# Kernel tuning notes

Hardware: AMD Instinct MI355X
Metric: run time of the kernel (lower is better)

## Reference

```python
import jax, jax.numpy as jnp
import numpy as np

D_MODEL, D_STATE, D_CONV, EXPAND, DT_RANK = 1024, 16, 4, 2, 64
D_INNER = EXPAND * D_MODEL
B, L = 2, 4096


def setup_inputs() -> dict:
    key = jax.random.key(0)
    ks = jax.random.split(key, 9)
    s = 0.02
    x = jax.random.normal(ks[0], (B, L, D_MODEL), dtype=jnp.float32)
    in_proj_w = jax.random.normal(ks[1], (D_MODEL, 2 * D_INNER), dtype=jnp.float32) * s
    conv_w = jax.random.normal(ks[2], (D_INNER, 1, D_CONV), dtype=jnp.float32) * s
    conv_b = jnp.zeros((D_INNER,), dtype=jnp.float32)
    x_proj_w = jax.random.normal(ks[3], (D_INNER, DT_RANK + 2 * D_STATE), dtype=jnp.float32) * s
    dt_proj_w = jax.random.normal(ks[4], (DT_RANK, D_INNER), dtype=jnp.float32) * s
    # dt bias -> softplus(dt) roughly in [1e-3, 1e-1] as in mamba init
    dt = jnp.exp(jax.random.uniform(ks[5], (D_INNER,)) * (np.log(0.1) - np.log(1e-3)) + np.log(1e-3))
    dt_proj_b = (dt + jnp.log(-jnp.expm1(-dt))).astype(jnp.float32)  # inverse softplus
    A_log = jnp.log(jnp.broadcast_to(jnp.arange(1, D_STATE + 1, dtype=jnp.float32), (D_INNER, D_STATE)))
    Dp = jnp.ones((D_INNER,), dtype=jnp.float32)
    out_proj_w = jax.random.normal(ks[6], (D_INNER, D_MODEL), dtype=jnp.float32) * s
    return {"x": x, "in_proj_w": in_proj_w, "conv_w": conv_w, "conv_b": conv_b,
            "x_proj_w": x_proj_w, "dt_proj_w": dt_proj_w, "dt_proj_b": dt_proj_b,
            "A_log": A_log, "Dp": Dp, "out_proj_w": out_proj_w}


def _mamba(x, in_proj_w, conv_w, conv_b, x_proj_w, dt_proj_w, dt_proj_b, A_log, Dp, out_proj_w):
    # in projection -> (u, z), each [B, L, D_INNER]
    xz = jnp.einsum('bld,de->ble', x, in_proj_w)
    u, z = jnp.split(xz, 2, axis=-1)
    # causal depthwise conv1d over time
    u_c = jax.lax.conv_general_dilated(
        u.transpose(0, 2, 1), conv_w, window_strides=(1,),
        padding=[(D_CONV - 1, 0)],
        dimension_numbers=('NCH', 'OIH', 'NCH'),
        feature_group_count=D_INNER)
    u_c = jax.nn.silu(u_c.transpose(0, 2, 1) + conv_b)  # [B, L, D_INNER]
    # input-dependent dt, B, C
    dbc = jnp.einsum('bld,dr->blr', u_c, x_proj_w)
    dt_lo, Bc, Cc = jnp.split(dbc, [DT_RANK, DT_RANK + D_STATE], axis=-1)
    dt = jax.nn.softplus(jnp.einsum('blr,rd->bld', dt_lo, dt_proj_w) + dt_proj_b)  # [B,L,Di]
    A = -jnp.exp(A_log)  # [Di, N]

    def step(h, inp):
        u_t, dt_t, B_t, C_t = inp  # [B,Di],[B,Di],[B,N],[B,N]
        dA = jnp.exp(dt_t[..., None] * A)                      # [B,Di,N]
        h = h * dA + (dt_t * u_t)[..., None] * B_t[:, None, :]  # [B,Di,N]
        y = jnp.einsum('bdn,bn->bd', h, C_t)                   # [B,Di]
        return h, y

    h0 = jnp.zeros((x.shape[0], D_INNER, D_STATE), dtype=x.dtype)
    xs = (u_c.transpose(1, 0, 2), dt.transpose(1, 0, 2),
          Bc.transpose(1, 0, 2), Cc.transpose(1, 0, 2))
    _, ys = jax.lax.scan(step, h0, xs)      # [L, B, Di]
    y = ys.transpose(1, 0, 2) + u_c * Dp    # skip connection
    y = y * jax.nn.silu(z)                  # gate
    return jnp.einsum('bld,de->ble', y, out_proj_w)


def reference(x, in_proj_w, conv_w, conv_b, x_proj_w, dt_proj_w, dt_proj_b, A_log, Dp, out_proj_w):
    return _mamba(x, in_proj_w, conv_w, conv_b, x_proj_w, dt_proj_w, dt_proj_b, A_log, Dp, out_proj_w)
```

## Files before the change

kernel.cpp:

```cpp
#include <hip/hip_runtime.h>
#include <hip/hip_bf16.h>
#include <math.h>

#define BSZ 2
#define LSEQ 4096
#define DMODEL 1024
#define DINNER 2048
#define NSTATE 16
#define DTRANK 64
#define MROWS (BSZ * LSEQ)
#define NCHUNK 64
#define CHUNK (LSEQ / NCHUNK)
#define XKS 8
#define XKCH (DINNER / XKS)

#if __has_builtin(__builtin_amdgcn_exp2f)
#define EXP2F(x) __builtin_amdgcn_exp2f(x)
#else
#define EXP2F(x) exp2f(x)
#endif
#define LOG2E 1.44269504088896f

typedef __attribute__((ext_vector_type(8))) short bf16x8;
typedef __attribute__((ext_vector_type(4))) float f32x4;

__device__ __forceinline__ float sigmoidf_(float x) { return 1.0f / (1.0f + __expf(-x)); }

__device__ __forceinline__ unsigned short f2bf(float x) {
    unsigned int u = __float_as_uint(x);
    u += 0x7fff + ((u >> 16) & 1);
    return (unsigned short)(u >> 16);
}
__device__ __forceinline__ float bf2f(unsigned short b) {
    return __uint_as_float(((unsigned int)b) << 16);
}

__global__ __launch_bounds__(256) void prep_kernel(
    const float* __restrict__ x, unsigned short* __restrict__ xbf,
    const float* __restrict__ w_in, unsigned short* __restrict__ wT_in,
    const float* __restrict__ w_out, unsigned short* __restrict__ wT_out,
    const float* __restrict__ w_x, unsigned short* __restrict__ wXT,
    const float* __restrict__ w_dt, unsigned short* __restrict__ wDT)
{
    __shared__ float tile[64][65];
    const int id = blockIdx.x;
    const int t = threadIdx.x;

    if (id >= 1632) {
        int gid = (id - 1632) * 256 + t;
        int m = gid >> 7;
        int g = gid & 127;
        size_t src = (size_t)m * 1024 + g * 8;
        float4 v0 = *reinterpret_cast<const float4*>(x + src);
        float4 v1 = *reinterpret_cast<const float4*>(x + src + 4);
        uint4 w;
        w.x = (unsigned)f2bf(v0.x) | ((unsigned)f2bf(v0.y) << 16);
        w.y = (unsigned)f2bf(v0.z) | ((unsigned)f2bf(v0.w) << 16);
        w.z = (unsigned)f2bf(v1.x) | ((unsigned)f2bf(v1.y) << 16);
        w.w = (unsigned)f2bf(v1.z) | ((unsigned)f2bf(v1.w) << 16);
        size_t dst = (size_t)m * 1024 + ((g * 8) ^ ((m & 7) << 3));
        *reinterpret_cast<uint4*>(xbf + dst) = w;
        return;
    }

    const float* W; unsigned short* WT; int K, Nsrc, nb, kb;
    if (id < 1024)      { W = w_in;  WT = wT_in;  K = 1024; Nsrc = 4096; nb = id & 63; kb = id >> 6; }
    else if (id < 1536) { int q = id - 1024; W = w_out; WT = wT_out; K = 2048; Nsrc = 1024; nb = q & 15; kb = q >> 4; }
    else if (id < 1600) { int q = id - 1536; W = w_x;   WT = wXT;   K = 2048; Nsrc = 96;   nb = q & 1;  kb = q >> 1; }
    else                { int q = id - 1600; W = w_dt;  WT = wDT;   K = 64;   Nsrc = 2048; nb = q;      kb = 0; }

    const int n0 = nb * 64;
    const int k0 = kb * 64;

    #pragma unroll
    for (int i = 0; i < 16; ++i) {
        int flat = i * 256 + t;
        int r = flat >> 6, c = flat & 63;
        tile[r][c] = (n0 + c < Nsrc) ? W[(size_t)(k0 + r) * Nsrc + n0 + c] : 0.0f;
    }
    __syncthreads();
    #pragma unroll
    for (int i = 0; i < 16; ++i) {
        int flat = i * 256 + t;
        int n = flat >> 6, k = flat & 63;
        int ks = k ^ ((n & 7) << 3);
        WT[(size_t)(n0 + n) * K + k0 + ks] = f2bf(tile[k][n]);
    }
}

template<int OBF>
__global__ __launch_bounds__(512) void gemm_bb512_kernel(
    const unsigned short* __restrict__ Abf, const unsigned short* __restrict__ BT,
    void* __restrict__ Cv, int M, int N, int K, int ldc)
{
    __shared__ unsigned short lds_a[128 * 64];
    __shared__ unsigned short lds_b[128 * 64];

    const int tid  = threadIdx.x;
    const int lane = tid & 63;
    const int w    = tid >> 6;
    const int wr   = (w >> 2) * 64;
    const int wc   = (w & 3) * 32;
    const int row0 = blockIdx.y * 128;
    const int col0 = blockIdx.x * 128;

    f32x4 acc[4][2];
    #pragma unroll
    for (int m = 0; m < 4; ++m)
        #pragma unroll
        for (int n = 0; n < 2; ++n)
            acc[m][n] = (f32x4){0.f, 0.f, 0.f, 0.f};

    for (int k0 = 0; k0 < K; k0 += 64) {
        #pragma unroll
        for (int j = 0; j < 2; ++j) {
            int c  = j * 512 + tid;
            int r  = c >> 3;
            int cc = c & 7;
            const char* asrc = (const char*)Abf +
                ((size_t)(row0 + r) * K + k0) * 2 + cc * 16;
            __builtin_amdgcn_global_load_lds(
                (const __attribute__((address_space(1))) void*)asrc,
                (__attribute__((address_space(3))) void*)((char*)lds_a + c * 16),
                16, 0, 0);
            const char* bsrc = (const char*)BT +
                ((size_t)(col0 + r) * K + k0) * 2 + cc * 16;
            __builtin_amdgcn_global_load_lds(
                (const __attribute__((address_space(1))) void*)bsrc,
                (__attribute__((address_space(3))) void*)((char*)lds_b + c * 16),
                16, 0, 0);
        }
        __syncthreads();

        #pragma unroll
        for (int kk = 0; kk < 2; ++kk) {
            bf16x8 af[4], bfr[2];
            #pragma unroll
            for (int m = 0; m < 4; ++m) {
                int r = wr + m * 16 + (lane & 15);
                int byteoff = r * 128 + ((kk * 64 + (lane >> 4) * 16) ^ ((r & 7) << 4));
                af[m] = *reinterpret_cast<const bf16x8*>((const char*)lds_a + byteoff);
            }
            #pragma unroll
            for (int n = 0; n < 2; ++n) {
                int r = wc + n * 16 + (lane & 15);
                int byteoff = r * 128 + ((kk * 64 + (lane >> 4) * 16) ^ ((r & 7) << 4));
                bfr[n] = *reinterpret_cast<const bf16x8*>((const char*)lds_b + byteoff);
            }
            #pragma unroll
            for (int m = 0; m < 4; ++m)
                #pragma unroll
                for (int n = 0; n < 2; ++n)
                    acc[m][n] = __builtin_amdgcn_mfma_f32_16x16x32_bf16(
                        af[m], bfr[n], acc[m][n], 0, 0, 0);
        }
        __syncthreads();
    }

    #pragma unroll
    for (int m = 0; m < 4; ++m) {
        int rbase = row0 + wr + m * 16 + (lane >> 4) * 4;
        #pragma unroll
        for (int n = 0; n < 2; ++n) {
            int col = col0 + wc + n * 16 + (lane & 15);
            #pragma unroll
            for (int r = 0; r < 4; ++r) {
                if (OBF) {
                    ((unsigned short*)Cv)[(size_t)(rbase + r) * ldc + col] =
                        f2bf(acc[m][n][r]);
                } else {
                    ((float*)Cv)[(size_t)(rbase + r) * ldc + col] = acc[m][n][r];
                }
            }
        }
    }
}

__global__ __launch_bounds__(256) void xproj_splitk_bb_kernel(
    const unsigned short* __restrict__ Abf, const unsigned short* __restrict__ BT,
    float* __restrict__ part)
{
    __shared__ unsigned short lds_a[128 * 64];
    __shared__ unsigned short lds_b[128 * 64];

    const int tid  = threadIdx.x;
    const int lane = tid & 63;
    const int w    = tid >> 6;
    const int wr   = (w >> 1) * 64;
    const int wc   = (w & 1) * 64;
    const int row0 = blockIdx.y * 128;
    const int kb   = blockIdx.z * XKCH;
    const int K    = DINNER;

    f32x4 acc[4][4];
    #pragma unroll
    for (int m = 0; m < 4; ++m)
        #pragma unroll
        for (int n = 0; n < 4; ++n)
            acc[m][n] = (f32x4){0.f, 0.f, 0.f, 0.f};

    for (int k0 = kb; k0 < kb + XKCH; k0 += 64) {
        #pragma unroll
        for (int j = 0; j < 4; ++j) {
            int c  = (j * 4 + w) * 64 + lane;
            int r  = c >> 3;
            int cc = c & 7;
            const char* asrc = (const char*)Abf +
                ((size_t)(row0 + r) * K + k0) * 2 + cc * 16;
            __builtin_amdgcn_global_load_lds(
                (const __attribute__((address_space(1))) void*)asrc,
                (__attribute__((address_space(3))) void*)((char*)lds_a + (j * 4 + w) * 1024),
                16, 0, 0);
            const char* bsrc = (const char*)BT +
                ((size_t)r * K + k0) * 2 + cc * 16;
            __builtin_amdgcn_global_load_lds(
                (const __attribute__((address_space(1))) void*)bsrc,
                (__attribute__((address_space(3))) void*)((char*)lds_b + (j * 4 + w) * 1024),
                16, 0, 0);
        }
        __syncthreads();

        #pragma unroll
        for (int kk = 0; kk < 2; ++kk) {
            bf16x8 af[4], bfr[4];
            #pragma unroll
            for (int m = 0; m < 4; ++m) {
                int r = wr + m * 16 + (lane & 15);
                int byteoff = r * 128 + ((kk * 64 + (lane >> 4) * 16) ^ ((r & 7) << 4));
                af[m] = *reinterpret_cast<const bf16x8*>((const char*)lds_a + byteoff);
            }
            #pragma unroll
            for (int n = 0; n < 4; ++n) {
                int r = wc + n * 16 + (lane & 15);
                int byteoff = r * 128 + ((kk * 64 + (lane >> 4) * 16) ^ ((r & 7) << 4));
                bfr[n] = *reinterpret_cast<const bf16x8*>((const char*)lds_b + byteoff);
            }
            #pragma unroll
            for (int m = 0; m < 4; ++m)
                #pragma unroll
                for (int n = 0; n < 4; ++n)
                    acc[m][n] = __builtin_amdgcn_mfma_f32_16x16x32_bf16(
                        af[m], bfr[n], acc[m][n], 0, 0, 0);
        }
        __syncthreads();
    }

    float* pbase = part + (size_t)blockIdx.z * MROWS * 96;
    #pragma unroll
    for (int m = 0; m < 4; ++m) {
        int rbase = row0 + wr + m * 16 + (lane >> 4) * 4;
        #pragma unroll
        for (int n = 0; n < 4; ++n) {
            int col = wc + n * 16 + (lane & 15);
            if (col < 96) {
                #pragma unroll
                for (int r = 0; r < 4; ++r)
                    pbase[(size_t)(rbase + r) * 96 + col] = acc[m][n][r];
            }
        }
    }
}

__global__ __launch_bounds__(256) void xproj_reduce_kernel(
    const float* __restrict__ part, float* __restrict__ dbc,
    unsigned short* __restrict__ dtlo)
{
    int gid = blockIdx.x * 256 + threadIdx.x;
    float s = 0.f;
    #pragma unroll
    for (int k = 0; k < XKS; ++k)
        s += part[(size_t)k * MROWS * 96 + gid];
    dbc[gid] = s;
    int row = gid / 96;
    int col = gid - row * 96;
    if (col < 64)
        dtlo[(size_t)row * 64 + (col ^ ((row & 7) << 3))] = f2bf(s);
}

__global__ __launch_bounds__(256) void gemm_dtproj_bb_kernel(
    const unsigned short* __restrict__ Abf, const unsigned short* __restrict__ BT,
    const float* __restrict__ bias, unsigned short* __restrict__ C)
{
    __shared__ unsigned short lds_a[128 * 64];
    __shared__ unsigned short lds_b[128 * 64];

    const int tid  = threadIdx.x;
    const int lane = tid & 63;
    const int w    = tid >> 6;
    const int wr   = (w >> 1) * 64;
    const int wc   = (w & 1) * 64;
    const int row0 = blockIdx.y * 128;
    const int col0 = blockIdx.x * 128;

    f32x4 acc[4][4];
    #pragma unroll
    for (int m = 0; m < 4; ++m)
        #pragma unroll
        for (int n = 0; n < 4; ++n)
            acc[m][n] = (f32x4){0.f, 0.f, 0.f, 0.f};

    #pragma unroll
    for (int j = 0; j < 4; ++j) {
        int c  = (j * 4 + w) * 64 + lane;
        int r  = c >> 3;
        int cc = c & 7;
        const char* asrc = (const char*)Abf + ((size_t)(row0 + r) * 64) * 2 + cc * 16;
        __builtin_amdgcn_global_load_lds(
            (const __attribute__((address_space(1))) void*)asrc,
            (__attribute__((address_space(3))) void*)((char*)lds_a + (j * 4 + w) * 1024),
            16, 0, 0);
        const char* bsrc = (const char*)BT + ((size_t)(col0 + r) * 64) * 2 + cc * 16;
        __builtin_amdgcn_global_load_lds(
            (const __attribute__((address_space(1))) void*)bsrc,
            (__attribute__((address_space(3))) void*)((char*)lds_b + (j * 4 + w) * 1024),
            16, 0, 0);
    }
    __syncthreads();

    #pragma unroll
    for (int kk = 0; kk < 2; ++kk) {
        bf16x8 af[4], bfr[4];
        #pragma unroll
        for (int m = 0; m < 4; ++m) {
            int r = wr + m * 16 + (lane & 15);
            int byteoff = r * 128 + ((kk * 64 + (lane >> 4) * 16) ^ ((r & 7) << 4));
            af[m] = *reinterpret_cast<const bf16x8*>((const char*)lds_a + byteoff);
        }
        #pragma unroll
        for (int n = 0; n < 4; ++n) {
            int r = wc + n * 16 + (lane & 15);
            int byteoff = r * 128 + ((kk * 64 + (lane >> 4) * 16) ^ ((r & 7) << 4));
            bfr[n] = *reinterpret_cast<const bf16x8*>((const char*)lds_b + byteoff);
        }
        #pragma unroll
        for (int m = 0; m < 4; ++m)
            #pragma unroll
            for (int n = 0; n < 4; ++n)
                acc[m][n] = __builtin_amdgcn_mfma_f32_16x16x32_bf16(
                    af[m], bfr[n], acc[m][n], 0, 0, 0);
    }

    #pragma unroll
    for (int m = 0; m < 4; ++m) {
        int rbase = row0 + wr + m * 16 + (lane >> 4) * 4;
        #pragma unroll
        for (int n = 0; n < 4; ++n) {
            int col = col0 + wc + n * 16 + (lane & 15);
            float bv = bias[col];
            #pragma unroll
            for (int r = 0; r < 4; ++r) {
                float v = acc[m][n][r] + bv;
                v = (v > 20.0f) ? v : log1pf(__expf(v));
                C[(size_t)(rbase + r) * DINNER + col] = f2bf(v);
            }
        }
    }
}

__global__ __launch_bounds__(256) void conv_silu_kernel(
    const unsigned short* __restrict__ xzb, const float* __restrict__ cw,
    const float* __restrict__ cb, unsigned short* __restrict__ ucbf)
{
    int gid = blockIdx.x * 256 + threadIdx.x;
    int row = gid >> 8;
    int d0  = (gid & 255) * 8;
    int t = row & (LSEQ - 1);

    uint4 uv[4];
    #pragma unroll
    for (int k = 0; k < 4; ++k) {
        if (t - 3 + k >= 0)
            uv[k] = *reinterpret_cast<const uint4*>(
                xzb + (size_t)(row + k - 3) * 4096 + d0);
        else
            uv[k] = (uint4){0u, 0u, 0u, 0u};
    }

    float v[8];
    #pragma unroll
    for (int i = 0; i < 8; ++i) {
        float acc = cb[d0 + i];
        float4 wv = *reinterpret_cast<const float4*>(cw + (size_t)(d0 + i) * 4);
        float wk[4] = {wv.x, wv.y, wv.z, wv.w};
        #pragma unroll
        for (int k = 0; k < 4; ++k) {
            unsigned int word = (&uv[k].x)[i >> 1];
            float u = __uint_as_float((i & 1) ? (word & 0xffff0000u) : (word << 16));
            acc = fmaf(u, wk[k], acc);
        }
        v[i] = acc * sigmoidf_(acc);
    }

    uint4 o;
    o.x = (unsigned)f2bf(v[0]) | ((unsigned)f2bf(v[1]) << 16);
    o.y = (unsigned)f2bf(v[2]) | ((unsigned)f2bf(v[3]) << 16);
    o.z = (unsigned)f2bf(v[4]) | ((unsigned)f2bf(v[5]) << 16);
    o.w = (unsigned)f2bf(v[6]) | ((unsigned)f2bf(v[7]) << 16);
    *reinterpret_cast<uint4*>(
        ucbf + (size_t)row * DINNER + (d0 ^ ((row & 7) << 3))) = o;
}

__global__ __launch_bounds__(256) void scan_partial_kernel(
    const unsigned short* __restrict__ dtb, const unsigned short* __restrict__ ucbf,
    const float* __restrict__ dbc, const float* __restrict__ A_log,
    float* __restrict__ Pbuf, float* __restrict__ Ebuf)
{
    __shared__ float sB[CHUNK][NSTATE];
    const int tid = threadIdx.x;
    const int c = blockIdx.x;
    const int b = blockIdx.z;
    const int d = blockIdx.y * 256 + tid;
    const size_t row0 = (size_t)b * LSEQ + c * CHUNK;

    {
        int s = tid >> 2, f = tid & 3;
        float4 v = *reinterpret_cast<const float4*>(dbc + (row0 + s) * 96 + 64 + f * 4);
        *reinterpret_cast<float4*>(&sB[s][f * 4]) = v;
    }

    float An2[NSTATE];
    #pragma unroll
    for (int k = 0; k < 4; ++k) {
        float4 a = *reinterpret_cast<const float4*>(A_log + (size_t)d * NSTATE + k * 4);
        An2[k*4+0] = -__expf(a.x) * LOG2E;
        An2[k*4+1] = -__expf(a.y) * LOG2E;
        An2[k*4+2] = -__expf(a.z) * LOG2E;
        An2[k*4+3] = -__expf(a.w) * LOG2E;
    }
    const float c0 = An2[0];
    bool powok = true;
    #pragma unroll
    for (int n = 1; n < NSTATE; ++n)
        powok = powok && (fabsf(An2[n] - (n + 1) * c0) <= 1e-4f * (n + 1) * fabsf(c0));
    __syncthreads();

    float E[NSTATE];
    #pragma unroll
    for (int n = 0; n < NSTATE; ++n) E[n] = 0.f;
    float S = 0.f;

    float dtc = bf2f(dtb[row0 * DINNER + d]);
    float ucv = bf2f(ucbf[row0 * DINNER + d]);
    for (int s = 0; s < CHUNK; ++s) {
        float dtn = 0.f, un = 0.f;
        if (s + 1 < CHUNK) {
            dtn = bf2f(dtb[(row0 + s + 1) * DINNER + d]);
            un  = bf2f(ucbf[(row0 + s + 1) * DINNER + (d ^ (((s + 1) & 7) << 3))]);
        }
        S += dtc;
        float du = dtc * ucv;
        float Bv[NSTATE];
        #pragma unroll
        for (int k = 0; k < 4; ++k)
            *reinterpret_cast<float4*>(&Bv[k*4]) =
                *reinterpret_cast<const float4*>(&sB[s][k*4]);
        if (powok) {
            float q = EXP2F(dtc * c0);
            float dA = q;
            #pragma unroll
            for (int n = 0; n < NSTATE; ++n) {
                E[n] = fmaf(E[n], dA, du * Bv[n]);
                dA *= q;
            }
        } else {
            #pragma unroll
            for (int n = 0; n < NSTATE; ++n) {
                float qq = EXP2F(dtc * An2[n]);
                E[n] = fmaf(E[n], qq, du * Bv[n]);
            }
        }
        dtc = dtn; ucv = un;
    }

    size_t base = (((size_t)c * BSZ + b) * DINNER + d) * NSTATE;
    if (powok) {
        float R = EXP2F(c0 * S);
        float P = R;
        #pragma unroll
        for (int n = 0; n < NSTATE; ++n) {
            Pbuf[base + n] = P;
            Ebuf[base + n] = E[n];
            P *= R;
        }
    } else {
        #pragma unroll
        for (int n = 0; n < NSTATE; ++n) {
            Pbuf[base + n] = EXP2F(An2[n] * S);
            Ebuf[base + n] = E[n];
        }
    }
}

__global__ __launch_bounds__(256) void scan_prefix_kernel(
    float* __restrict__ Pbuf, const float* __restrict__ Ebuf)
{
    const int gid = blockIdx.x * 256 + threadIdx.x;
    const size_t stride = (size_t)BSZ * DINNER * NSTATE;
    size_t idx = gid;
    float h = 0.f;
    for (int c = 0; c < NCHUNK; ++c) {
        float P = Pbuf[idx];
        float Ev = Ebuf[idx];
        Pbuf[idx] = h;
        h = fmaf(P, h, Ev);
        idx += stride;
    }
}

__global__ __launch_bounds__(256) void scan_final_kernel(
    const unsigned short* __restrict__ dtb, const unsigned short* __restrict__ ucbf,
    const unsigned short* __restrict__ xzb, const float* __restrict__ dbc,
    const float* __restrict__ A_log, const float* __restrict__ Dp,
    const float* __restrict__ H0, unsigned short* __restrict__ ybf)
{
    __shared__ float sBC[CHUNK][2 * NSTATE];
    const int tid = threadIdx.x;
    const int c = blockIdx.x;
    const int b = blockIdx.z;
    const int d = blockIdx.y * 256 + tid;
    const size_t row0 = (size_t)b * LSEQ + c * CHUNK;

    {
        #pragma unroll
        for (int i = 0; i < 2; ++i) {
            int j = tid * 2 + i;
            int s = j >> 3, f = j & 7;
            float4 v = *reinterpret_cast<const float4*>(dbc + (row0 + s) * 96 + 64 + f * 4);
            *reinterpret_cast<float4*>(&sBC[s][f * 4]) = v;
        }
    }

    float An2[NSTATE];
    #pragma unroll
    for (int k = 0; k < 4; ++k) {
        float4 a = *reinterpret_cast<const float4*>(A_log + (size_t)d * NSTATE + k * 4);
        An2[k*4+0] = -__expf(a.x) * LOG2E;
        An2[k*4+1] = -__expf(a.y) * LOG2E;
        An2[k*4+2] = -__expf(a.z) * LOG2E;
        An2[k*4+3] = -__expf(a.w) * LOG2E;
    }
    const float c0 = An2[0];
    bool powok = true;
    #pragma unroll
    for (int n = 1; n < NSTATE; ++n)
        powok = powok && (fabsf(An2[n] - (n + 1) * c0) <= 1e-4f * (n + 1) * fabsf(c0));
    const float Dpd = Dp[d];

    float h[NSTATE];
    {
        size_t base = (((size_t)c * BSZ + b) * DINNER + d) * NSTATE;
        #pragma unroll
        for (int n = 0; n < NSTATE; ++n) h[n] = H0[base + n];
    }
    __syncthreads();

    float dtc = bf2f(dtb[row0 * DINNER + d]);
    float ucv = bf2f(ucbf[row0 * DINNER + d]);
    float zc  = bf2f(xzb[row0 * 4096 + 2048 + d]);
    for (int s = 0; s < CHUNK; ++s) {
        float dtn = 0.f, un = 0.f, zn = 0.f;
        if (s + 1 < CHUNK) {
            dtn = bf2f(dtb[(row0 + s + 1) * DINNER + d]);
            un  = bf2f(ucbf[(row0 + s + 1) * DINNER + (d ^ (((s + 1) & 7) << 3))]);
            zn  = bf2f(xzb[(row0 + s + 1) * 4096 + 2048 + d]);
        }
        float du = dtc * ucv;
        float Bv[NSTATE], Cv[NSTATE];
        #pragma unroll
        for (int k = 0; k < 4; ++k) {
            *reinterpret_cast<float4*>(&Bv[k*4]) =
                *reinterpret_cast<const float4*>(&sBC[s][k*4]);
            *reinterpret_cast<float4*>(&Cv[k*4]) =
                *reinterpret_cast<const float4*>(&sBC[s][16 + k*4]);
        }
        float y0 = 0.f, y1 = 0.f, y2 = 0.f, y3 = 0.f;
        if (powok) {
            float q = EXP2F(dtc * c0);
            float dA = q;
            #pragma unroll
            for (int n = 0; n < NSTATE; ++n) {
                h[n] = fmaf(h[n], dA, du * Bv[n]);
                float& yk = (n & 3) == 0 ? y0 : (n & 3) == 1 ? y1 : (n & 3) == 2 ? y2 : y3;
                yk = fmaf(h[n], Cv[n], yk);
                dA *= q;
            }
        } else {
            #pragma unroll
            for (int n = 0; n < NSTATE; ++n) {
                float qq = EXP2F(dtc * An2[n]);
                h[n] = fmaf(h[n], qq, du * Bv[n]);
                float& yk = (n & 3) == 0 ? y0 : (n & 3) == 1 ? y1 : (n & 3) == 2 ? y2 : y3;
                yk = fmaf(h[n], Cv[n], yk);
            }
        }
        float y = (y0 + y1) + (y2 + y3);
        float yg = (y + ucv * Dpd) * (zc * sigmoidf_(zc));
        ybf[(row0 + s) * DINNER + (d ^ ((s & 7) << 3))] = f2bf(yg);
        dtc = dtn; ucv = un; zc = zn;
    }
}

extern "C" void kernel_launch(void* const* d_in, const int* in_sizes, int n_in,
                              void* d_out, int out_size, void* d_ws, size_t ws_size,
                              hipStream_t stream)
{
    const float* x         = (const float*)d_in[0];
    const float* in_proj_w = (const float*)d_in[1];
    const float* conv_w    = (const float*)d_in[2];
    const float* conv_b    = (const float*)d_in[3];
    const float* x_proj_w  = (const float*)d_in[4];
    const float* dt_proj_w = (const float*)d_in[5];
    const float* dt_proj_b = (const float*)d_in[6];
    const float* A_log     = (const float*)d_in[7];
    const float* Dp        = (const float*)d_in[8];
    const float* out_proj_w= (const float*)d_in[9];
    float* out = (float*)d_out;

    char* base = (char*)d_ws;
    unsigned short* xzb  = (unsigned short*)base;
    unsigned short* dtb  = (unsigned short*)(base + (64ull << 20));
    unsigned short* ucbf = (unsigned short*)(base + (96ull << 20));
    float* dbc           = (float*)(base + (128ull << 20));
    unsigned short* wT_in  = (unsigned short*)(base + (131ull << 20));
    unsigned short* wT_out = (unsigned short*)(base + (139ull << 20));
    unsigned short* wXT    = (unsigned short*)(base + (143ull << 20));
    unsigned short* wDT    = (unsigned short*)(base + (143ull << 20) + (512ull << 10));
    char* U = base + (144ull << 20);
    unsigned short* xbf  = (unsigned short*)U;
    float* part          = (float*)U;
    unsigned short* dtlo = (unsigned short*)(U + (24ull << 20));
    float* Pbuf          = (float*)U;
    float* Ebuf          = (float*)(U + (16ull << 20));
    unsigned short* ybf  = (unsigned short*)(U + (32ull << 20));

    dim3 blk(256);
    dim3 blk512(512);

    prep_kernel<<<dim3(5728), blk, 0, stream>>>(
        x, xbf, in_proj_w, wT_in, out_proj_w, wT_out, x_proj_w, wXT, dt_proj_w, wDT);

    gemm_bb512_kernel<1><<<dim3(32, 64), blk512, 0, stream>>>(
        xbf, wT_in, (void*)xzb, MROWS, 4096, 1024, 4096);

    conv_silu_kernel<<<dim3((MROWS * (DINNER / 8)) / 256), blk, 0, stream>>>(
        xzb, conv_w, conv_b, ucbf);

    xproj_splitk_bb_kernel<<<dim3(1, 64, XKS), blk, 0, stream>>>(ucbf, wXT, part);
    xproj_reduce_kernel<<<dim3((MROWS * 96) / 256), blk, 0, stream>>>(part, dbc, dtlo);

    gemm_dtproj_bb_kernel<<<dim3(16, 64), blk, 0, stream>>>(dtlo, wDT, dt_proj_b, dtb);

    scan_partial_kernel<<<dim3(NCHUNK, DINNER / 256, BSZ), blk, 0, stream>>>(
        dtb, ucbf, dbc, A_log, Pbuf, Ebuf);
    scan_prefix_kernel<<<dim3((BSZ * DINNER * NSTATE) / 256), blk, 0, stream>>>(Pbuf, Ebuf);
    scan_final_kernel<<<dim3(NCHUNK, DINNER / 256, BSZ), blk, 0, stream>>>(
        dtb, ucbf, xzb, dbc, A_log, Dp, Pbuf, ybf);

    gemm_bb512_kernel<0><<<dim3(8, 64), blk512, 0, stream>>>(
        ybf, wT_out, (void*)out, MROWS, 1024, 2048, 1024);
}
```

Measured before the change: 373.9 us.

## Batch-prefetch scan inputs in groups and widen xproj GEMM to 512 threads

The three scan kernels now load the next group of time steps (8 or 4 values of dt, u, z, or P/E) into registers while the current group is computed. Before, only one step was prefetched ahead, so more memory loads can now be in flight to hide global-memory latency. The xproj split-K GEMM moves from 4 to 8 waves per block, each wave computing a 64x32 tile instead of 64x64, which adds waves per block for latency hiding. The cost is higher register pressure in the scan kernels, which could lower occupancy.

New measurement: 390.0 us. 1.04x slower.

```diff
diff --git a/kernel.cpp b/kernel.cpp
--- a/kernel.cpp
+++ b/kernel.cpp
@@ -176,7 +176,7 @@
     }
 }
 
-__global__ __launch_bounds__(256) void xproj_splitk_bb_kernel(
+__global__ __launch_bounds__(512) void xproj_splitk_bb512_kernel(
     const unsigned short* __restrict__ Abf, const unsigned short* __restrict__ BT,
     float* __restrict__ part)
 {
@@ -186,43 +186,43 @@
     const int tid  = threadIdx.x;
     const int lane = tid & 63;
     const int w    = tid >> 6;
-    const int wr   = (w >> 1) * 64;
-    const int wc   = (w & 1) * 64;
+    const int wr   = (w >> 2) * 64;
+    const int wc   = (w & 3) * 32;
     const int row0 = blockIdx.y * 128;
     const int kb   = blockIdx.z * XKCH;
     const int K    = DINNER;
 
-    f32x4 acc[4][4];
+    f32x4 acc[4][2];
     #pragma unroll
     for (int m = 0; m < 4; ++m)
         #pragma unroll
-        for (int n = 0; n < 4; ++n)
+        for (int n = 0; n < 2; ++n)
             acc[m][n] = (f32x4){0.f, 0.f, 0.f, 0.f};
 
     for (int k0 = kb; k0 < kb + XKCH; k0 += 64) {
         #pragma unroll
-        for (int j = 0; j < 4; ++j) {
-            int c  = (j * 4 + w) * 64 + lane;
+        for (int j = 0; j < 2; ++j) {
+            int c  = j * 512 + tid;
             int r  = c >> 3;
             int cc = c & 7;
             const char* asrc = (const char*)Abf +
                 ((size_t)(row0 + r) * K + k0) * 2 + cc * 16;
             __builtin_amdgcn_global_load_lds(
                 (const __attribute__((address_space(1))) void*)asrc,
-                (__attribute__((address_space(3))) void*)((char*)lds_a + (j * 4 + w) * 1024),
+                (__attribute__((address_space(3))) void*)((char*)lds_a + c * 16),
                 16, 0, 0);
             const char* bsrc = (const char*)BT +
                 ((size_t)r * K + k0) * 2 + cc * 16;
             __builtin_amdgcn_global_load_lds(
                 (const __attribute__((address_space(1))) void*)bsrc,
-                (__attribute__((address_space(3))) void*)((char*)lds_b + (j * 4 + w) * 1024),
+                (__attribute__((address_space(3))) void*)((char*)lds_b + c * 16),
                 16, 0, 0);
         }
         __syncthreads();
 
         #pragma unroll
         for (int kk = 0; kk < 2; ++kk) {
-            bf16x8 af[4], bfr[4];
+            bf16x8 af[4], bfr[2];
             #pragma unroll
             for (int m = 0; m < 4; ++m) {
                 int r = wr + m * 16 + (lane & 15);
@@ -230,7 +230,7 @@
                 af[m] = *reinterpret_cast<const bf16x8*>((const char*)lds_a + byteoff);
             }
             #pragma unroll
-            for (int n = 0; n < 4; ++n) {
+            for (int n = 0; n < 2; ++n) {
                 int r = wc + n * 16 + (lane & 15);
                 int byteoff = r * 128 + ((kk * 64 + (lane >> 4) * 16) ^ ((r & 7) << 4));
                 bfr[n] = *reinterpret_cast<const bf16x8*>((const char*)lds_b + byteoff);
@@ -238,7 +238,7 @@
             #pragma unroll
             for (int m = 0; m < 4; ++m)
                 #pragma unroll
-                for (int n = 0; n < 4; ++n)
+                for (int n = 0; n < 2; ++n)
                     acc[m][n] = __builtin_amdgcn_mfma_f32_16x16x32_bf16(
                         af[m], bfr[n], acc[m][n], 0, 0, 0);
         }
@@ -250,7 +250,7 @@
     for (int m = 0; m < 4; ++m) {
         int rbase = row0 + wr + m * 16 + (lane >> 4) * 4;
         #pragma unroll
-        for (int n = 0; n < 4; ++n) {
+        for (int n = 0; n < 2; ++n) {
             int col = wc + n * 16 + (lane & 15);
             if (col < 96) {
                 #pragma unroll
@@ -439,37 +439,51 @@
     for (int n = 0; n < NSTATE; ++n) E[n] = 0.f;
     float S = 0.f;
 
-    float dtc = bf2f(dtb[row0 * DINNER + d]);
-    float ucv = bf2f(ucbf[row0 * DINNER + d]);
-    for (int s = 0; s < CHUNK; ++s) {
-        float dtn = 0.f, un = 0.f;
-        if (s + 1 < CHUNK) {
-            dtn = bf2f(dtb[(row0 + s + 1) * DINNER + d]);
-            un  = bf2f(ucbf[(row0 + s + 1) * DINNER + (d ^ (((s + 1) & 7) << 3))]);
-        }
-        S += dtc;
-        float du = dtc * ucv;
-        float Bv[NSTATE];
-        #pragma unroll
-        for (int k = 0; k < 4; ++k)
-            *reinterpret_cast<float4*>(&Bv[k*4]) =
-                *reinterpret_cast<const float4*>(&sB[s][k*4]);
-        if (powok) {
-            float q = EXP2F(dtc * c0);
-            float dA = q;
-            #pragma unroll
-            for (int n = 0; n < NSTATE; ++n) {
-                E[n] = fmaf(E[n], dA, du * Bv[n]);
-                dA *= q;
-            }
-        } else {
-            #pragma unroll
-            for (int n = 0; n < NSTATE; ++n) {
-                float qq = EXP2F(dtc * An2[n]);
-                E[n] = fmaf(E[n], qq, du * Bv[n]);
-            }
-        }
-        dtc = dtn; ucv = un;
+    float dtv[8], uv[8];
+    #pragma unroll
+    for (int i = 0; i < 8; ++i) {
+        dtv[i] = bf2f(dtb[(row0 + i) * DINNER + d]);
+        uv[i]  = bf2f(ucbf[(row0 + i) * DINNER + (d ^ (i << 3))]);
+    }
+
+    for (int g = 0; g < 8; ++g) {
+        float dtn[8], un[8];
+        if (g < 7) {
+            #pragma unroll
+            for (int i = 0; i < 8; ++i) {
+                int s = (g + 1) * 8 + i;
+                dtn[i] = bf2f(dtb[(row0 + s) * DINNER + d]);
+                un[i]  = bf2f(ucbf[(row0 + s) * DINNER + (d ^ (i << 3))]);
+            }
+        }
+        #pragma unroll
+        for (int i = 0; i < 8; ++i) {
+            int s = g * 8 + i;
+            S += dtv[i];
+            float du = dtv[i] * uv[i];
+            float Bv[NSTATE];
+            #pragma unroll
+            for (int k = 0; k < 4; ++k)
+                *reinterpret_cast<float4*>(&Bv[k*4]) =
+                    *reinterpret_cast<const float4*>(&sB[s][k*4]);
+            if (powok) {
+                float q = EXP2F(dtv[i] * c0);
+                float dA = q;
+                #pragma unroll
+                for (int n = 0; n < NSTATE; ++n) {
+                    E[n] = fmaf(E[n], dA, du * Bv[n]);
+                    dA *= q;
+                }
+            } else {
+                #pragma unroll
+                for (int n = 0; n < NSTATE; ++n) {
+                    float qq = EXP2F(dtv[i] * An2[n]);
+                    E[n] = fmaf(E[n], qq, du * Bv[n]);
+                }
+            }
+        }
+        #pragma unroll
+        for (int i = 0; i < 8; ++i) { dtv[i] = dtn[i]; uv[i] = un[i]; }
     }
 
     size_t base = (((size_t)c * BSZ + b) * DINNER + d) * NSTATE;
@@ -498,12 +512,31 @@
     const size_t stride = (size_t)BSZ * DINNER * NSTATE;
     size_t idx = gid;
     float h = 0.f;
-    for (int c = 0; c < NCHUNK; ++c) {
-        float P = Pbuf[idx];
-        float Ev = Ebuf[idx];
-        Pbuf[idx] = h;
-        h = fmaf(P, h, Ev);
-        idx += stride;
+
+    float Pv[8], Ev[8];
+    #pragma unroll
+    for (int i = 0; i < 8; ++i) {
+        Pv[i] = Pbuf[idx + (size_t)i * stride];
+        Ev[i] = Ebuf[idx + (size_t)i * stride];
+    }
+    for (int g = 0; g < 8; ++g) {
+        float Pn[8], En[8];
+        if (g < 7) {
+            size_t nb = idx + (size_t)8 * stride;
+            #pragma unroll
+            for (int i = 0; i < 8; ++i) {
+                Pn[i] = Pbuf[nb + (size_t)i * stride];
+                En[i] = Ebuf[nb + (size_t)i * stride];
+            }
+        }
+        #pragma unroll
+        for (int i = 0; i < 8; ++i) {
+            Pbuf[idx + (size_t)i * stride] = h;
+            h = fmaf(Pv[i], h, Ev[i]);
+        }
+        idx += (size_t)8 * stride;
+        #pragma unroll
+        for (int i = 0; i < 8; ++i) { Pv[i] = Pn[i]; Ev[i] = En[i]; }
     }
 }
 
@@ -554,49 +587,65 @@
     }
     __syncthreads();
 
-    float dtc = bf2f(dtb[row0 * DINNER + d]);
-    float ucv = bf2f(ucbf[row0 * DINNER + d]);
-    float zc  = bf2f(xzb[row0 * 4096 + 2048 + d]);
-    for (int s = 0; s < CHUNK; ++s) {
-        float dtn = 0.f, un = 0.f, zn = 0.f;
-        if (s + 1 < CHUNK) {
-            dtn = bf2f(dtb[(row0 + s + 1) * DINNER + d]);
-            un  = bf2f(ucbf[(row0 + s + 1) * DINNER + (d ^ (((s + 1) & 7) << 3))]);
-            zn  = bf2f(xzb[(row0 + s + 1) * 4096 + 2048 + d]);
-        }
-        float du = dtc * ucv;
-        float Bv[NSTATE], Cv[NSTATE];
-        #pragma unroll
-        for (int k = 0; k < 4; ++k) {
-            *reinterpret_cast<float4*>(&Bv[k*4]) =
-                *reinterpret_cast<const float4*>(&sBC[s][k*4]);
-            *reinterpret_cast<float4*>(&Cv[k*4]) =
-                *reinterpret_cast<const float4*>(&sBC[s][16 + k*4]);
-        }
-        float y0 = 0.f, y1 = 0.f, y2 = 0.f, y3 = 0.f;
-        if (powok) {
-            float q = EXP2F(dtc * c0);
-            float dA = q;
-            #pragma unroll
-            for (int n = 0; n < NSTATE; ++n) {
-                h[n] = fmaf(h[n], dA, du * Bv[n]);
-                float& yk = (n & 3) == 0 ? y0 : (n & 3) == 1 ? y1 : (n & 3) == 2 ? y2 : y3;
-                yk = fmaf(h[n], Cv[n], yk);
-                dA *= q;
-            }
-        } else {
-            #pragma unroll
-            for (int n = 0; n < NSTATE; ++n) {
-                float qq = EXP2F(dtc * An2[n]);
-                h[n] = fmaf(h[n], qq, du * Bv[n]);
-                float& yk = (n & 3) == 0 ? y0 : (n & 3) == 1 ? y1 : (n & 3) == 2 ? y2 : y3;
-                yk = fmaf(h[n], Cv[n], yk);
-            }
-        }
-        float y = (y0 + y1) + (y2 + y3);
-        float yg = (y + ucv * Dpd) * (zc * sigmoidf_(zc));
-        ybf[(row0 + s) * DINNER + (d ^ ((s & 7) << 3))] = f2bf(yg);
-        dtc = dtn; ucv = un; zc = zn;
+    float dtv[4], uv[4], zv[4];
+    #pragma unroll
+    for (int i = 0; i < 4; ++i) {
+        dtv[i] = bf2f(dtb[(row0 + i) * DINNER + d]);
+        uv[i]  = bf2f(ucbf[(row0 + i) * DINNER + (d ^ (i << 3))]);
+        zv[i]  = bf2f(xzb[(row0 + i) * 4096 + 2048 + d]);
+    }
+
+    for (int g = 0; g < 16; ++g) {
+        float dtn[4], un[4], zn[4];
+        if (g < 15) {
+            int xo = (((g + 1) & 1) << 2);
+            #pragma unroll
+            for (int i = 0; i < 4; ++i) {
+                int s = (g + 1) * 4 + i;
+                dtn[i] = bf2f(dtb[(row0 + s) * DINNER + d]);
+                un[i]  = bf2f(ucbf[(row0 + s) * DINNER + (d ^ ((xo + i) << 3))]);
+                zn[i]  = bf2f(xzb[(row0 + s) * 4096 + 2048 + d]);
+            }
+        }
+        int xg = ((g & 1) << 2);
+        #pragma unroll
+        for (int i = 0; i < 4; ++i) {
+            int s = g * 4 + i;
+            float du = dtv[i] * uv[i];
+            float Bv[NSTATE], Cv[NSTATE];
+            #pragma unroll
+            for (int k = 0; k < 4; ++k) {
+                *reinterpret_cast<float4*>(&Bv[k*4]) =
+                    *reinterpret_cast<const float4*>(&sBC[s][k*4]);
+                *reinterpret_cast<float4*>(&Cv[k*4]) =
+                    *reinterpret_cast<const float4*>(&sBC[s][16 + k*4]);
+            }
+            float y0 = 0.f, y1 = 0.f, y2 = 0.f, y3 = 0.f;
+            if (powok) {
+                float q = EXP2F(dtv[i] * c0);
+                float dA = q;
+                #pragma unroll
+                for (int n = 0; n < NSTATE; ++n) {
+                    h[n] = fmaf(h[n], dA, du * Bv[n]);
+                    float& yk = (n & 3) == 0 ? y0 : (n & 3) == 1 ? y1 : (n & 3) == 2 ? y2 : y3;
+                    yk = fmaf(h[n], Cv[n], yk);
+                    dA *= q;
+                }
+            } else {
+                #pragma unroll
+                for (int n = 0; n < NSTATE; ++n) {
+                    float qq = EXP2F(dtv[i] * An2[n]);
+                    h[n] = fmaf(h[n], qq, du * Bv[n]);
+                    float& yk = (n & 3) == 0 ? y0 : (n & 3) == 1 ? y1 : (n & 3) == 2 ? y2 : y3;
+                    yk = fmaf(h[n], Cv[n], yk);
+                }
+            }
+            float y = (y0 + y1) + (y2 + y3);
+            float yg = (y + uv[i] * Dpd) * (zv[i] * sigmoidf_(zv[i]));
+            ybf[(row0 + s) * DINNER + (d ^ ((xg + i) << 3))] = f2bf(yg);
+        }
+        #pragma unroll
+        for (int i = 0; i < 4; ++i) { dtv[i] = dtn[i]; uv[i] = un[i]; zv[i] = zn[i]; }
     }
 }
 
@@ -645,7 +694,7 @@
     conv_silu_kernel<<<dim3((MROWS * (DINNER / 8)) / 256), blk, 0, stream>>>(
         xzb, conv_w, conv_b, ucbf);
 
-    xproj_splitk_bb_kernel<<<dim3(1, 64, XKS), blk, 0, stream>>>(ucbf, wXT, part);
+    xproj_splitk_bb512_kernel<<<dim3(1, 64, XKS), blk512, 0, stream>>>(ucbf, wXT, part);
     xproj_reduce_kernel<<<dim3((MROWS * 96) / 256), blk, 0, stream>>>(part, dbc, dtlo);
 
     gemm_dtproj_bb_kernel<<<dim3(16, 64), blk, 0, stream>>>(dtlo, wDT, dt_proj_b, dtb);
```
